# Kernel optimization log

Hardware: AMD Instinct MI355X
Metric: run time of the kernel (lower is better)

## Reference

```python
import jax, jax.numpy as jnp
import numpy as np

HIDDEN, FFN, N_EXPERTS, TOP_K = 1024, 4096, 8, 2


def setup_inputs() -> dict:
    key = jax.random.key(0)
    ks = jax.random.split(key, 8)
    s_h = 1.0 / np.sqrt(HIDDEN)
    s_f = 1.0 / np.sqrt(FFN)
    return {
        "x": jax.random.normal(ks[0], (1, 1024, HIDDEN), dtype=jnp.float32),
        "gate_w": jax.random.normal(ks[1], (N_EXPERTS, HIDDEN), dtype=jnp.float32) * s_h,
        "gate_b": jnp.zeros((N_EXPERTS,), dtype=jnp.float32),
        "w1": jax.random.normal(ks[2], (N_EXPERTS, HIDDEN, FFN), dtype=jnp.float32) * s_h,
        "b1": jnp.zeros((N_EXPERTS, FFN), dtype=jnp.float32),
        "w2": jax.random.normal(ks[3], (N_EXPERTS, FFN, HIDDEN), dtype=jnp.float32) * s_f,
        "b2": jnp.zeros((N_EXPERTS, HIDDEN), dtype=jnp.float32),
    }


def reference(x, gate_w, gate_b, w1, b1, w2, b2):
    B, S, H = x.shape
    x_flat = x.reshape(-1, H)  # (T, H)
    # Router: top-k gating with softmax over selected logits
    logits = x_flat @ gate_w.T + gate_b  # (T, E)
    top_w, sel = jax.lax.top_k(logits, TOP_K)  # (T, K)
    rw = jax.nn.softmax(top_w, axis=-1)  # (T, K)
    # combine[t, e] = router weight of expert e for token t (0 if not selected)
    combine = jnp.sum(jax.nn.one_hot(sel, N_EXPERTS, dtype=x.dtype) * rw[..., None], axis=1)  # (T, E)
    # Dense all-expert FFN, combined with routing weights (zero weight => zero contribution,
    # identical math to the masked gather/scatter loop in the torch module)
    h = jax.nn.gelu(jnp.einsum('th,ehf->tef', x_flat, w1) + b1, approximate=False)  # (T, E, F)
    y = jnp.einsum('tef,efh->teh', h, w2) + b2  # (T, E, H)
    out = jnp.einsum('te,teh->th', combine, y)  # (T, H)
    return out.reshape(B, S, H)
```

## Files before the change

### kernel.cpp

```cpp
#include <hip/hip_runtime.h>


typedef __bf16 bf16;
typedef __bf16 bf16x8 __attribute__((ext_vector_type(8)));
typedef float floatx4 __attribute__((ext_vector_type(4)));

#define T_TOK 1024
#define HID 1024
#define FFN 4096
#define NEXP 8
#define BM 128
#define BN 128
#define BK 32

__device__ __forceinline__ void llds16(const void* g, void* l) {
  __builtin_amdgcn_global_load_lds((const __attribute__((address_space(1))) void*)g,
                                   (__attribute__((address_space(3))) void*)l, 16, 0, 0);
}

__global__ void xconv_k(const float* __restrict__ x, bf16* __restrict__ xb) {
  int i = blockIdx.x * 256 + threadIdx.x;
  float4 a = ((const float4*)x)[i * 2];
  float4 b = ((const float4*)x)[i * 2 + 1];
  bf16 t[8] = {(bf16)a.x, (bf16)a.y, (bf16)a.z, (bf16)a.w,
               (bf16)b.x, (bf16)b.y, (bf16)b.z, (bf16)b.w};
  *(bf16x8*)&xb[(size_t)i * 8] = *(bf16x8*)t;
}

__global__ void transconv_k(const float* __restrict__ in0, bf16* __restrict__ out0,
                            int R, int C) {
  const size_t eoff = (size_t)blockIdx.z * R * C;
  const float* in = in0 + eoff;
  bf16* out = out0 + eoff;
  int c = blockIdx.x * 256 + threadIdx.x;
  int r0 = blockIdx.y * 64;
#pragma unroll
  for (int jb = 0; jb < 8; jb++) {
    float v[8];
    bf16 b[8];
#pragma unroll
    for (int j = 0; j < 8; j++) v[j] = in[(size_t)(r0 + jb * 8 + j) * C + c];
#pragma unroll
    for (int j = 0; j < 8; j++) b[j] = (bf16)v[j];
    *(bf16x8*)&out[(size_t)c * R + r0 + jb * 8] = *(bf16x8*)b;
  }
}

__global__ void router_k(const float* __restrict__ x, const float* __restrict__ gw,
                         const float* __restrict__ gb, int* __restrict__ cnt,
                         int* __restrict__ elist, float* __restrict__ ewt) {
  int wave = threadIdx.x >> 6;
  int lane = threadIdx.x & 63;
  int t = blockIdx.x * 4 + wave;
  const float* xr = x + (size_t)t * HID;
  float xv[16];
#pragma unroll
  for (int j = 0; j < 16; j++) xv[j] = xr[lane + 64 * j];
  float logits[NEXP];
#pragma unroll
  for (int e = 0; e < NEXP; e++) {
    const float* g = gw + (size_t)e * HID;
    float s = 0.f;
#pragma unroll
    for (int j = 0; j < 16; j++) s += xv[j] * g[lane + 64 * j];
#pragma unroll
    for (int off = 32; off; off >>= 1) s += __shfl_xor(s, off, 64);
    logits[e] = s + gb[e];
  }
  int i0 = 0; float l0 = logits[0];
#pragma unroll
  for (int e = 1; e < NEXP; e++) if (logits[e] > l0) { l0 = logits[e]; i0 = e; }
  int i1 = -1; float l1 = -3.0e38f;
#pragma unroll
  for (int e = 0; e < NEXP; e++) if (e != i0 && logits[e] > l1) { l1 = logits[e]; i1 = e; }
  if (lane == 0) {
    float w0 = 1.f / (1.f + expf(l1 - l0));
    float w1 = 1.f - w0;
    int p0 = atomicAdd(cnt + i0, 1);
    elist[i0 * T_TOK + p0] = t * 2 + 0; ewt[i0 * T_TOK + p0] = w0;
    int p1 = atomicAdd(cnt + i1, 1);
    elist[i1 * T_TOK + p1] = t * 2 + 1; ewt[i1 * T_TOK + p1] = w1;
  }
}

__global__ void gemm1_k(const bf16* __restrict__ xb, const bf16* __restrict__ w1t,
                        const float* __restrict__ b1, const int* __restrict__ cnt,
                        const int* __restrict__ elist, bf16* __restrict__ hbuf) {
  int e = blockIdx.z;
  int c = cnt[e];
  int m0 = blockIdx.y * BM;
  if (m0 >= c) return;
  int n0 = blockIdx.x * BN;

  __shared__ __align__(16) bf16 As[BM][BK];
  __shared__ __align__(16) bf16 Bs[BN][BK];

  int tid = threadIdx.x;
  int wv = tid >> 6, ln = tid & 63;
  int lrow = wv * 16 + (ln >> 2);
  int lk8 = (ln & 3) * 8;

  int ra0 = m0 + lrow;      if (ra0 >= c) ra0 = c - 1;
  int ra1 = m0 + lrow + 64; if (ra1 >= c) ra1 = c - 1;
  const bf16* ap0 = xb + (size_t)(elist[e * T_TOK + ra0] >> 1) * HID + lk8;
  const bf16* ap1 = xb + (size_t)(elist[e * T_TOK + ra1] >> 1) * HID + lk8;
  const bf16* w1e = w1t + (size_t)e * FFN * HID;
  const bf16* bp0 = w1e + (size_t)(n0 + lrow) * HID + lk8;
  const bf16* bp1 = bp0 + (size_t)64 * HID;
  bf16* ad0 = &As[wv * 16][0];
  bf16* ad1 = &As[64 + wv * 16][0];
  bf16* bd0 = &Bs[wv * 16][0];
  bf16* bd1 = &Bs[64 + wv * 16][0];

  floatx4 acc[4][4] = {};
  int fm = ln & 15, quad = ln >> 4;
  int wm = (wv & 1) * 64, wn = (wv >> 1) * 64;

  for (int k0 = 0; k0 < HID; k0 += BK) {
    llds16(ap0, ad0); llds16(ap1, ad1);
    llds16(bp0, bd0); llds16(bp1, bd1);
    ap0 += BK; ap1 += BK; bp0 += BK; bp1 += BK;
    __syncthreads();
    bf16x8 af[4], bfr[4];
#pragma unroll
    for (int i = 0; i < 4; i++) af[i] = *(const bf16x8*)&As[wm + i * 16 + fm][quad * 8];
#pragma unroll
    for (int j = 0; j < 4; j++) bfr[j] = *(const bf16x8*)&Bs[wn + j * 16 + fm][quad * 8];
#pragma unroll
    for (int i = 0; i < 4; i++)
#pragma unroll
      for (int j = 0; j < 4; j++)
        acc[i][j] = __builtin_amdgcn_mfma_f32_16x16x32_bf16(af[i], bfr[j], acc[i][j], 0, 0, 0);
    __syncthreads();
  }

  const float* b1e = b1 + (size_t)e * FFN;
#pragma unroll
  for (int i = 0; i < 4; i++) {
    int rb = m0 + wm + i * 16 + quad * 4;
#pragma unroll
    for (int j = 0; j < 4; j++) {
      int col = n0 + wn + j * 16 + fm;
      float bias = b1e[col];
#pragma unroll
      for (int r = 0; r < 4; r++) {
        int row = rb + r;
        if (row < c) {
          int slot = elist[e * T_TOK + row];
          float v = acc[i][j][r] + bias;
          float g = 0.5f * v * (1.f + erff(v * 0.70710678118654752f));
          hbuf[(size_t)slot * FFN + col] = (bf16)g;
        }
      }
    }
  }
}

__global__ void gemm2_k(const bf16* __restrict__ hbuf, const bf16* __restrict__ w2t,
                        const float* __restrict__ b2, const int* __restrict__ cnt,
                        const int* __restrict__ elist, const float* __restrict__ ewt,
                        float* __restrict__ part) {
  int e = blockIdx.z & 7;
  int ks = blockIdx.z >> 3;
  int c = cnt[e];
  int m0 = blockIdx.y * BM;
  if (m0 >= c) return;
  int n0 = blockIdx.x * BN;
  int kbeg = ks * (FFN / 4);

  __shared__ __align__(16) bf16 As[BM][BK];
  __shared__ __align__(16) bf16 Bs[BN][BK];

  int tid = threadIdx.x;
  int wv = tid >> 6, ln = tid & 63;
  int lrow = wv * 16 + (ln >> 2);
  int lk8 = (ln & 3) * 8;

  int ra0 = m0 + lrow;      if (ra0 >= c) ra0 = c - 1;
  int ra1 = m0 + lrow + 64; if (ra1 >= c) ra1 = c - 1;
  const bf16* ap0 = hbuf + (size_t)elist[e * T_TOK + ra0] * FFN + kbeg + lk8;
  const bf16* ap1 = hbuf + (size_t)elist[e * T_TOK + ra1] * FFN + kbeg + lk8;
  const bf16* w2e = w2t + (size_t)e * HID * FFN;
  const bf16* bp0 = w2e + (size_t)(n0 + lrow) * FFN + kbeg + lk8;
  const bf16* bp1 = bp0 + (size_t)64 * FFN;
  bf16* ad0 = &As[wv * 16][0];
  bf16* ad1 = &As[64 + wv * 16][0];
  bf16* bd0 = &Bs[wv * 16][0];
  bf16* bd1 = &Bs[64 + wv * 16][0];

  floatx4 acc[4][4] = {};
  int fm = ln & 15, quad = ln >> 4;
  int wm = (wv & 1) * 64, wn = (wv >> 1) * 64;

  for (int it = 0; it < (FFN / 4) / BK; it++) {
    llds16(ap0, ad0); llds16(ap1, ad1);
    llds16(bp0, bd0); llds16(bp1, bd1);
    ap0 += BK; ap1 += BK; bp0 += BK; bp1 += BK;
    __syncthreads();
    bf16x8 af[4], bfr[4];
#pragma unroll
    for (int i = 0; i < 4; i++) af[i] = *(const bf16x8*)&As[wm + i * 16 + fm][quad * 8];
#pragma unroll
    for (int j = 0; j < 4; j++) bfr[j] = *(const bf16x8*)&Bs[wn + j * 16 + fm][quad * 8];
#pragma unroll
    for (int i = 0; i < 4; i++)
#pragma unroll
      for (int j = 0; j < 4; j++)
        acc[i][j] = __builtin_amdgcn_mfma_f32_16x16x32_bf16(af[i], bfr[j], acc[i][j], 0, 0, 0);
    __syncthreads();
  }

  const float* b2e = b2 + (size_t)e * HID;
#pragma unroll
  for (int i = 0; i < 4; i++) {
    int rb = m0 + wm + i * 16 + quad * 4;
#pragma unroll
    for (int j = 0; j < 4; j++) {
      int col = n0 + wn + j * 16 + fm;
      float bias = (ks == 0) ? b2e[col] : 0.f;
#pragma unroll
      for (int r = 0; r < 4; r++) {
        int row = rb + r;
        if (row < c) {
          int slot = elist[e * T_TOK + row];
          float w = ewt[e * T_TOK + row];
          part[((size_t)ks * (2 * T_TOK) + slot) * HID + col] = w * (acc[i][j][r] + bias);
        }
      }
    }
  }
}

__global__ void combine_k(const float* __restrict__ part, float* __restrict__ out) {
  int i = blockIdx.x * 256 + threadIdx.x;
  int t = i >> 8;
  int h4 = (i & 255) * 4;
  float4 s = {0.f, 0.f, 0.f, 0.f};
#pragma unroll
  for (int ks = 0; ks < 4; ks++)
#pragma unroll
    for (int sl = 0; sl < 2; sl++) {
      float4 v = *(const float4*)&part[((size_t)ks * (2 * T_TOK) + t * 2 + sl) * HID + h4];
      s.x += v.x; s.y += v.y; s.z += v.z; s.w += v.w;
    }
  *(float4*)&out[(size_t)t * HID + h4] = s;
}

extern "C" void kernel_launch(void* const* d_in, const int* in_sizes, int n_in,
                              void* d_out, int out_size, void* d_ws, size_t ws_size,
                              hipStream_t stream) {
  const float* x  = (const float*)d_in[0];
  const float* gw = (const float*)d_in[1];
  const float* gb = (const float*)d_in[2];
  const float* w1 = (const float*)d_in[3];
  const float* b1 = (const float*)d_in[4];
  const float* w2 = (const float*)d_in[5];
  const float* b2 = (const float*)d_in[6];
  float* out = (float*)d_out;

  char* ws = (char*)d_ws;
  int*   cnt   = (int*)ws;
  int*   elist = (int*)(ws + 1024);
  float* ewt   = (float*)(ws + 1024 + 32768);
  bf16*  xb    = (bf16*)(ws + (1 << 16));
  bf16*  wt    = (bf16*)(ws + ((size_t)4 << 20));
  size_t hoff  = ((size_t)4 << 20) + (size_t)NEXP * FFN * HID * 2;
  bf16*  hbuf  = (bf16*)(ws + hoff);
  float* part  = (float*)(ws + hoff + (size_t)(2 * T_TOK) * FFN * 2);

  hipMemsetAsync(cnt, 0, 32, stream);
  xconv_k<<<512, 256, 0, stream>>>(x, xb);
  router_k<<<T_TOK / 4, 256, 0, stream>>>(x, gw, gb, cnt, elist, ewt);
  transconv_k<<<dim3(FFN / 256, HID / 64, NEXP), 256, 0, stream>>>(w1, wt, HID, FFN);
  gemm1_k<<<dim3(FFN / BN, 8, NEXP), 256, 0, stream>>>(xb, wt, b1, cnt, elist, hbuf);
  transconv_k<<<dim3(HID / 256, FFN / 64, NEXP), 256, 0, stream>>>(w2, wt, FFN, HID);
  gemm2_k<<<dim3(HID / BN, 8, NEXP * 4), 256, 0, stream>>>(hbuf, wt, b2, cnt, elist, ewt, part);
  combine_k<<<(T_TOK * HID / 4) / 256, 256, 0, stream>>>(part, out);
}
```

Baseline: 532.8 us.

## Fuse fp32 weight conversion into expert GEMM tile loads, drop transpose kernels

Removes the separate transpose-and-convert kernels for w1 and w2 and instead has each GEMM load fp32 weights directly, converting to bf16 in registers and storing transposed into padded LDS tiles. Global loads are prefetched into registers one K-step ahead so they overlap the MFMA work. This eliminates a full write and re-read of a bf16 weight copy, at the cost of the same weight tile being read in fp32 by multiple M blocks and extra conversion work inside the GEMM.

```diff
diff --git a/kernel.cpp b/kernel.cpp
--- a/kernel.cpp
+++ b/kernel.cpp
@@ -12,11 +12,7 @@
 #define BM 128
 #define BN 128
 #define BK 32
-
-__device__ __forceinline__ void llds16(const void* g, void* l) {
-  __builtin_amdgcn_global_load_lds((const __attribute__((address_space(1))) void*)g,
-                                   (__attribute__((address_space(3))) void*)l, 16, 0, 0);
-}
+#define LP 36
 
 __global__ void xconv_k(const float* __restrict__ x, bf16* __restrict__ xb) {
   int i = blockIdx.x * 256 + threadIdx.x;
@@ -25,25 +21,6 @@
   bf16 t[8] = {(bf16)a.x, (bf16)a.y, (bf16)a.z, (bf16)a.w,
                (bf16)b.x, (bf16)b.y, (bf16)b.z, (bf16)b.w};
   *(bf16x8*)&xb[(size_t)i * 8] = *(bf16x8*)t;
-}
-
-__global__ void transconv_k(const float* __restrict__ in0, bf16* __restrict__ out0,
-                            int R, int C) {
-  const size_t eoff = (size_t)blockIdx.z * R * C;
-  const float* in = in0 + eoff;
-  bf16* out = out0 + eoff;
-  int c = blockIdx.x * 256 + threadIdx.x;
-  int r0 = blockIdx.y * 64;
-#pragma unroll
-  for (int jb = 0; jb < 8; jb++) {
-    float v[8];
-    bf16 b[8];
-#pragma unroll
-    for (int j = 0; j < 8; j++) v[j] = in[(size_t)(r0 + jb * 8 + j) * C + c];
-#pragma unroll
-    for (int j = 0; j < 8; j++) b[j] = (bf16)v[j];
-    *(bf16x8*)&out[(size_t)c * R + r0 + jb * 8] = *(bf16x8*)b;
-  }
 }
 
 __global__ void router_k(const float* __restrict__ x, const float* __restrict__ gw,
@@ -83,43 +60,58 @@
   }
 }
 
-__global__ void gemm1_k(const bf16* __restrict__ xb, const bf16* __restrict__ w1t,
-                        const float* __restrict__ b1, const int* __restrict__ cnt,
-                        const int* __restrict__ elist, bf16* __restrict__ hbuf) {
+__global__ __launch_bounds__(256)
+void gemm1_k(const bf16* __restrict__ xb, const float* __restrict__ w1,
+             const float* __restrict__ b1, const int* __restrict__ cnt,
+             const int* __restrict__ elist, bf16* __restrict__ hbuf) {
   int e = blockIdx.z;
   int c = cnt[e];
   int m0 = blockIdx.y * BM;
   if (m0 >= c) return;
   int n0 = blockIdx.x * BN;
 
-  __shared__ __align__(16) bf16 As[BM][BK];
-  __shared__ __align__(16) bf16 Bs[BN][BK];
+  __shared__ __align__(16) bf16 As[BM][LP];
+  __shared__ __align__(16) bf16 Bs[BN][LP];
 
   int tid = threadIdx.x;
-  int wv = tid >> 6, ln = tid & 63;
-  int lrow = wv * 16 + (ln >> 2);
-  int lk8 = (ln & 3) * 8;
-
-  int ra0 = m0 + lrow;      if (ra0 >= c) ra0 = c - 1;
-  int ra1 = m0 + lrow + 64; if (ra1 >= c) ra1 = c - 1;
-  const bf16* ap0 = xb + (size_t)(elist[e * T_TOK + ra0] >> 1) * HID + lk8;
-  const bf16* ap1 = xb + (size_t)(elist[e * T_TOK + ra1] >> 1) * HID + lk8;
-  const bf16* w1e = w1t + (size_t)e * FFN * HID;
-  const bf16* bp0 = w1e + (size_t)(n0 + lrow) * HID + lk8;
-  const bf16* bp1 = bp0 + (size_t)64 * HID;
-  bf16* ad0 = &As[wv * 16][0];
-  bf16* ad1 = &As[64 + wv * 16][0];
-  bf16* bd0 = &Bs[wv * 16][0];
-  bf16* bd1 = &Bs[64 + wv * 16][0];
+  int ar = tid >> 1;
+  int ac = (tid & 1) * 16;
+  int ra = m0 + ar; if (ra >= c) ra = c - 1;
+  const bf16* aptr = xb + (size_t)(elist[e * T_TOK + ra] >> 1) * HID + ac;
+  int bn = tid & 127;
+  int bk = (tid >> 7) * 16;
+  const float* bptr = w1 + (size_t)e * HID * FFN + (size_t)bk * FFN + n0 + bn;
+
+  uint4 a0, a1;
+  float bfl[16];
+  a0 = *(const uint4*)(aptr);
+  a1 = *(const uint4*)(aptr + 8);
+#pragma unroll
+  for (int j = 0; j < 16; j++) bfl[j] = bptr[(size_t)j * FFN];
 
   floatx4 acc[4][4] = {};
+  int ln = tid & 63, wv = tid >> 6;
   int fm = ln & 15, quad = ln >> 4;
   int wm = (wv & 1) * 64, wn = (wv >> 1) * 64;
 
-  for (int k0 = 0; k0 < HID; k0 += BK) {
-    llds16(ap0, ad0); llds16(ap1, ad1);
-    llds16(bp0, bd0); llds16(bp1, bd1);
-    ap0 += BK; ap1 += BK; bp0 += BK; bp1 += BK;
+  for (int t = 0; t < HID / BK; t++) {
+    bf16 bb[16];
+#pragma unroll
+    for (int j = 0; j < 16; j++) bb[j] = (bf16)bfl[j];
+    uint4 wa0 = a0, wa1 = a1;
+    __syncthreads();
+    *(uint4*)&As[ar][ac]      = wa0;
+    *(uint4*)&As[ar][ac + 8]  = wa1;
+    *(bf16x8*)&Bs[bn][bk]     = *(bf16x8*)&bb[0];
+    *(bf16x8*)&Bs[bn][bk + 8] = *(bf16x8*)&bb[8];
+    if (t + 1 < HID / BK) {
+      aptr += BK;
+      a0 = *(const uint4*)(aptr);
+      a1 = *(const uint4*)(aptr + 8);
+      bptr += (size_t)BK * FFN;
+#pragma unroll
+      for (int j = 0; j < 16; j++) bfl[j] = bptr[(size_t)j * FFN];
+    }
     __syncthreads();
     bf16x8 af[4], bfr[4];
 #pragma unroll
@@ -131,7 +123,6 @@
 #pragma unroll
       for (int j = 0; j < 4; j++)
         acc[i][j] = __builtin_amdgcn_mfma_f32_16x16x32_bf16(af[i], bfr[j], acc[i][j], 0, 0, 0);
-    __syncthreads();
   }
 
   const float* b1e = b1 + (size_t)e * FFN;
@@ -156,10 +147,11 @@
   }
 }
 
-__global__ void gemm2_k(const bf16* __restrict__ hbuf, const bf16* __restrict__ w2t,
-                        const float* __restrict__ b2, const int* __restrict__ cnt,
-                        const int* __restrict__ elist, const float* __restrict__ ewt,
-                        float* __restrict__ part) {
+__global__ __launch_bounds__(256)
+void gemm2_k(const bf16* __restrict__ hbuf, const float* __restrict__ w2,
+             const float* __restrict__ b2, const int* __restrict__ cnt,
+             const int* __restrict__ elist, const float* __restrict__ ewt,
+             float* __restrict__ part) {
   int e = blockIdx.z & 7;
   int ks = blockIdx.z >> 3;
   int c = cnt[e];
@@ -168,34 +160,49 @@
   int n0 = blockIdx.x * BN;
   int kbeg = ks * (FFN / 4);
 
-  __shared__ __align__(16) bf16 As[BM][BK];
-  __shared__ __align__(16) bf16 Bs[BN][BK];
+  __shared__ __align__(16) bf16 As[BM][LP];
+  __shared__ __align__(16) bf16 Bs[BN][LP];
 
   int tid = threadIdx.x;
-  int wv = tid >> 6, ln = tid & 63;
-  int lrow = wv * 16 + (ln >> 2);
-  int lk8 = (ln & 3) * 8;
-
-  int ra0 = m0 + lrow;      if (ra0 >= c) ra0 = c - 1;
-  int ra1 = m0 + lrow + 64; if (ra1 >= c) ra1 = c - 1;
-  const bf16* ap0 = hbuf + (size_t)elist[e * T_TOK + ra0] * FFN + kbeg + lk8;
-  const bf16* ap1 = hbuf + (size_t)elist[e * T_TOK + ra1] * FFN + kbeg + lk8;
-  const bf16* w2e = w2t + (size_t)e * HID * FFN;
-  const bf16* bp0 = w2e + (size_t)(n0 + lrow) * FFN + kbeg + lk8;
-  const bf16* bp1 = bp0 + (size_t)64 * FFN;
-  bf16* ad0 = &As[wv * 16][0];
-  bf16* ad1 = &As[64 + wv * 16][0];
-  bf16* bd0 = &Bs[wv * 16][0];
-  bf16* bd1 = &Bs[64 + wv * 16][0];
+  int ar = tid >> 1;
+  int ac = (tid & 1) * 16;
+  int ra = m0 + ar; if (ra >= c) ra = c - 1;
+  const bf16* aptr = hbuf + (size_t)elist[e * T_TOK + ra] * FFN + kbeg + ac;
+  int bn = tid & 127;
+  int bk = (tid >> 7) * 16;
+  const float* bptr = w2 + (size_t)e * FFN * HID + (size_t)(kbeg + bk) * HID + n0 + bn;
+
+  uint4 a0, a1;
+  float bfl[16];
+  a0 = *(const uint4*)(aptr);
+  a1 = *(const uint4*)(aptr + 8);
+#pragma unroll
+  for (int j = 0; j < 16; j++) bfl[j] = bptr[(size_t)j * HID];
 
   floatx4 acc[4][4] = {};
+  int ln = tid & 63, wv = tid >> 6;
   int fm = ln & 15, quad = ln >> 4;
   int wm = (wv & 1) * 64, wn = (wv >> 1) * 64;
 
-  for (int it = 0; it < (FFN / 4) / BK; it++) {
-    llds16(ap0, ad0); llds16(ap1, ad1);
-    llds16(bp0, bd0); llds16(bp1, bd1);
-    ap0 += BK; ap1 += BK; bp0 += BK; bp1 += BK;
+  const int NT = (FFN / 4) / BK;
+  for (int t = 0; t < NT; t++) {
+    bf16 bb[16];
+#pragma unroll
+    for (int j = 0; j < 16; j++) bb[j] = (bf16)bfl[j];
+    uint4 wa0 = a0, wa1 = a1;
+    __syncthreads();
+    *(uint4*)&As[ar][ac]      = wa0;
+    *(uint4*)&As[ar][ac + 8]  = wa1;
+    *(bf16x8*)&Bs[bn][bk]     = *(bf16x8*)&bb[0];
+    *(bf16x8*)&Bs[bn][bk + 8] = *(bf16x8*)&bb[8];
+    if (t + 1 < NT) {
+      aptr += BK;
+      a0 = *(const uint4*)(aptr);
+      a1 = *(const uint4*)(aptr + 8);
+      bptr += (size_t)BK * HID;
+#pragma unroll
+      for (int j = 0; j < 16; j++) bfl[j] = bptr[(size_t)j * HID];
+    }
     __syncthreads();
     bf16x8 af[4], bfr[4];
 #pragma unroll
@@ -207,7 +214,6 @@
 #pragma unroll
       for (int j = 0; j < 4; j++)
         acc[i][j] = __builtin_amdgcn_mfma_f32_16x16x32_bf16(af[i], bfr[j], acc[i][j], 0, 0, 0);
-    __syncthreads();
   }
 
   const float* b2e = b2 + (size_t)e * HID;
@@ -263,17 +269,13 @@
   int*   elist = (int*)(ws + 1024);
   float* ewt   = (float*)(ws + 1024 + 32768);
   bf16*  xb    = (bf16*)(ws + (1 << 16));
-  bf16*  wt    = (bf16*)(ws + ((size_t)4 << 20));
-  size_t hoff  = ((size_t)4 << 20) + (size_t)NEXP * FFN * HID * 2;
-  bf16*  hbuf  = (bf16*)(ws + hoff);
-  float* part  = (float*)(ws + hoff + (size_t)(2 * T_TOK) * FFN * 2);
+  bf16*  hbuf  = (bf16*)(ws + ((size_t)4 << 20));
+  float* part  = (float*)(ws + ((size_t)24 << 20));
 
   hipMemsetAsync(cnt, 0, 32, stream);
   xconv_k<<<512, 256, 0, stream>>>(x, xb);
   router_k<<<T_TOK / 4, 256, 0, stream>>>(x, gw, gb, cnt, elist, ewt);
-  transconv_k<<<dim3(FFN / 256, HID / 64, NEXP), 256, 0, stream>>>(w1, wt, HID, FFN);
-  gemm1_k<<<dim3(FFN / BN, 8, NEXP), 256, 0, stream>>>(xb, wt, b1, cnt, elist, hbuf);
-  transconv_k<<<dim3(HID / 256, FFN / 64, NEXP), 256, 0, stream>>>(w2, wt, FFN, HID);
-  gemm2_k<<<dim3(HID / BN, 8, NEXP * 4), 256, 0, stream>>>(hbuf, wt, b2, cnt, elist, ewt, part);
+  gemm1_k<<<dim3(FFN / BN, 8, NEXP), 256, 0, stream>>>(xb, w1, b1, cnt, elist, hbuf);
+  gemm2_k<<<dim3(HID / BN, 8, NEXP * 4), 256, 0, stream>>>(hbuf, w2, b2, cnt, elist, ewt, part);
   combine_k<<<(T_TOK * HID / 4) / 256, 256, 0, stream>>>(part, out);
 }
```

New measurement: 436.2 us. 18.1% less time.
